# Kernel optimization log

Hardware: AMD Instinct MI355X
Metric: run time of the kernel (lower is better)

Reference implementation:

```python
import jax, jax.numpy as jnp
import numpy as np

PAST = 16
FUTURE = 4
DIM = 64
INPUT_SIZE = 256
NUM_LAYERS = 3
DILATION = [1, 2, 4, 8]
INPUT_LENGTH = 1024
BATCH = 16
NEG_INF = -1e9


def _dilated_masks(length, num_layers, dilation):
    # mask[i, t, s] == True means position t may NOT attend to position s in layer i.
    # Layer i attends to s = t - k*dilation[i] for k in [0, window) with
    # window = dilation[i+1] // dilation[i] (causal, dilated local window).
    idx = np.arange(length)
    diff = idx[:, None] - idx[None, :]  # t - s
    masks = []
    for i in range(num_layers):
        d = dilation[i]
        window = dilation[i + 1] // d
        allowed = (diff >= 0) & (diff % d == 0) & (diff < window * d)
        masks.append(~allowed)
    return jnp.asarray(np.stack(masks, 0))


def setup_inputs() -> dict:
    key = jax.random.key(0)
    k_inp, k_w, k_b = jax.random.split(key, 3)
    inp = jax.random.normal(k_inp, (BATCH, INPUT_LENGTH, INPUT_SIZE), dtype=jnp.float32)
    # BottleLinear(input_size, output_size): plain Linear over last dim
    out_size = FUTURE * DIM
    bound = 1.0 / np.sqrt(INPUT_SIZE)
    W_out = jax.random.uniform(k_w, (out_size, INPUT_SIZE), minval=-bound, maxval=bound, dtype=jnp.float32)
    b_out = jax.random.uniform(k_b, (out_size,), minval=-bound, maxval=bound, dtype=jnp.float32)
    masks = _dilated_masks(INPUT_LENGTH, NUM_LAYERS, DILATION)
    return {"inp": inp, "W_out": W_out, "b_out": b_out, "masks": masks}


def reference(inp, W_out, b_out, masks):
    # inp: [B, L, D]; masks: [num_layers, L, L] bool (True = masked)
    B, L, D = inp.shape
    scale = 1.0 / jnp.sqrt(jnp.asarray(D, inp.dtype))
    residual = inp[:, PAST:, :DIM][:, :, None, :]  # [B, L-past, 1, dim]
    out = inp
    attns = []
    for i in range(NUM_LAYERS):
        mask = masks[i, :L, :L]
        scores = jnp.einsum('bld,bmd->blm', out, out) * scale
        scores = jnp.where(mask[None], NEG_INF, scores)
        attn = jax.nn.softmax(scores, axis=-1)  # [B, L, L]
        # dropout=0.0 (eval); residual self-attention layer
        out = jnp.einsum('blm,bmd->bld', attn, out) + out
        attns.append(attn)
    o = out[:, PAST:]  # [B, L-past, D]
    o = jnp.einsum('bld,od->blo', o, W_out) + b_out
    o = o.reshape(B, L - PAST, FUTURE, DIM) + residual
    attn_stack = jnp.stack(attns, 1)  # [B, num_layers, L, L]
    return o, attn_stack
```

## Files before the change

### kernel.cpp

```cpp
#include <hip/hip_runtime.h>

#define BATCH 16
#define LEN 1024
#define DIN 256
#define PAST 16
#define OUTROWS (LEN - PAST)
#define NL 3
#define TROWS 32
#define HALO 8
#define NR (TROWS + HALO)
#define O_ELEMS ((size_t)BATCH * OUTROWS * 256)

typedef float f4_t __attribute__((ext_vector_type(4)));

__device__ __forceinline__ void layer_step(const float (*S)[DIN], float (*D)[DIN],
                                           const int DD, const int layer,
                                           const int b, const int l0,
                                           const int wave, const int lane,
                                           float* __restrict__ attn)
{
    #pragma unroll
    for (int it = 0; it < NR / 8; ++it) {
        const int row = it * 8 + wave;
        const int l   = l0 - HALO + row;
        const int ry  = (row >= DD) ? (row - DD) : 0;

        const float4 x = ((const float4*)(S[row]))[lane];
        const float4 y = ((const float4*)(S[ry]))[lane];

        float d0 = x.x * x.x + x.y * x.y + x.z * x.z + x.w * x.w;
        float d1 = x.x * y.x + x.y * y.y + x.z * y.z + x.w * y.w;
        #pragma unroll
        for (int off = 32; off; off >>= 1) {
            d0 += __shfl_xor(d0, off, 64);
            d1 += __shfl_xor(d1, off, 64);
        }

        float p0 = 1.f, p1 = 0.f;
        if (l >= DD) {
            const float s0 = d0 * 0.0625f, s1 = d1 * 0.0625f;
            const float m  = fmaxf(s0, s1);
            const float e0 = expf(s0 - m), e1 = expf(s1 - m);
            const float inv = 1.f / (e0 + e1);
            p0 = e0 * inv;
            p1 = e1 * inv;
        }

        const float a0 = 1.f + p0;
        float4 nv;
        nv.x = fmaf(y.x, p1, x.x * a0);
        nv.y = fmaf(y.y, p1, x.y * a0);
        nv.z = fmaf(y.z, p1, x.z * a0);
        nv.w = fmaf(y.w, p1, x.w * a0);
        ((float4*)(D[row]))[lane] = nv;

        if (row >= HALO) {
            float* arow = attn + (((size_t)(b * NL + layer)) * LEN + l) * (size_t)LEN;
            #pragma unroll
            for (int j = 0; j < 4; ++j) {
                const int col = j * 256 + lane * 4;
                float4 v = make_float4(0.f, 0.f, 0.f, 0.f);
                const int dd = l - col;
                if (dd >= 0 && dd < 4) ((float*)&v)[dd] = p0;
                if (l >= DD) {
                    const int dp = (l - DD) - col;
                    if (dp >= 0 && dp < 4) ((float*)&v)[dp] = p1;
                }
                __builtin_nontemporal_store(*(const f4_t*)&v,
                                            (f4_t*)arow + j * 64 + lane);
            }
        }
    }
}

__global__ __launch_bounds__(512, 4) void fused_kernel(const float* __restrict__ inp,
                                                       const float* __restrict__ W,
                                                       const float* __restrict__ bias,
                                                       float* __restrict__ o,
                                                       float* __restrict__ attn)
{
    __shared__ float A[NR][DIN];
    __shared__ float Bb[NR][DIN];

    const int blk  = blockIdx.x;
    const int b    = blk >> 5;
    const int l0   = (blk & 31) * TROWS;
    const int t    = threadIdx.x;
    const int wave = t >> 6;
    const int lane = t & 63;

    {
        float4* dst = (float4*)A;
        const size_t base = (size_t)b * LEN;
        #pragma unroll
        for (int i = 0; i < 5; ++i) {
            const int idx = i * 512 + t;
            const int row = idx >> 6;
            int g = l0 - HALO + row; if (g < 0) g = 0;
            dst[idx] = ((const float4*)(inp + (base + g) * DIN))[idx & 63];
        }
    }
    __syncthreads();

    layer_step(A,  Bb, 1, 0, b, l0, wave, lane, attn);
    __syncthreads();
    layer_step(Bb, A,  2, 1, b, l0, wave, lane, attn);
    __syncthreads();
    layer_step(A,  Bb, 4, 2, b, l0, wave, lane, attn);
    __syncthreads();

    const int half = t >> 8;
    const int c    = t & 255;
    float acc[16];
    #pragma unroll
    for (int r = 0; r < 16; ++r) acc[r] = 0.f;

    const float4* W4 = (const float4*)(W + (size_t)c * DIN);
    const float4* R4 = (const float4*)(Bb[HALO + half * 16]);
    for (int kq = 0; kq < 64; ++kq) {
        const float4 wv = W4[kq];
        #pragma unroll
        for (int r = 0; r < 16; ++r) {
            const float4 xr = R4[r * 64 + kq];
            acc[r] = fmaf(wv.x, xr.x, acc[r]);
            acc[r] = fmaf(wv.y, xr.y, acc[r]);
            acc[r] = fmaf(wv.z, xr.z, acc[r]);
            acc[r] = fmaf(wv.w, xr.w, acc[r]);
        }
    }

    const float bv   = bias[c];
    const int   dcol = c & 63;
    #pragma unroll
    for (int r = 0; r < 16; ++r) {
        const int l = l0 + half * 16 + r;
        if (l >= PAST) {
            const float res = inp[((size_t)b * LEN + l) * DIN + dcol];
            o[((size_t)b * OUTROWS + (l - PAST)) * 256 + c] = acc[r] + bv + res;
        }
    }
}

extern "C" void kernel_launch(void* const* d_in, const int* in_sizes, int n_in,
                              void* d_out, int out_size, void* d_ws, size_t ws_size,
                              hipStream_t stream) {
    const float* inp   = (const float*)d_in[0];
    const float* W_out = (const float*)d_in[1];
    const float* b_out = (const float*)d_in[2];

    float* o_out    = (float*)d_out;
    float* attn_out = o_out + O_ELEMS;

    fused_kernel<<<BATCH * (LEN / TROWS), 512, 0, stream>>>(inp, W_out, b_out,
                                                            o_out, attn_out);
}
```

Before: 303.6 us.

## Drop final barrier and retile output projection so each wave owns its rows

Turns layer_step into a template with compile-time dilation, layer and row range, and skips the first row group of the last layer because those halo rows feed no output. The output linear is retiled so each wave computes a 4-row by 4-column block only from rows it wrote itself. That lets the final __syncthreads be removed, and the output is written with vectorized non-temporal float4 stores. The cost is strided W loads across lanes (each lane reads four separate W rows), which may hurt coalescing compared with the old contiguous per-thread row reads.

After: 403.2 us. 32.8% more time.

```diff
diff --git a/kernel.cpp b/kernel.cpp
--- a/kernel.cpp
+++ b/kernel.cpp
@@ -13,14 +13,14 @@
 
 typedef float f4_t __attribute__((ext_vector_type(4)));
 
+template<int DD, int LAYER, int ITBEG, int ITEND>
 __device__ __forceinline__ void layer_step(const float (*S)[DIN], float (*D)[DIN],
-                                           const int DD, const int layer,
                                            const int b, const int l0,
                                            const int wave, const int lane,
                                            float* __restrict__ attn)
 {
     #pragma unroll
-    for (int it = 0; it < NR / 8; ++it) {
+    for (int it = ITBEG; it < ITEND; ++it) {
         const int row = it * 8 + wave;
         const int l   = l0 - HALO + row;
         const int ry  = (row >= DD) ? (row - DD) : 0;
@@ -55,7 +55,7 @@
         ((float4*)(D[row]))[lane] = nv;
 
         if (row >= HALO) {
-            float* arow = attn + (((size_t)(b * NL + layer)) * LEN + l) * (size_t)LEN;
+            float* arow = attn + (((size_t)(b * NL + LAYER)) * LEN + l) * (size_t)LEN;
             #pragma unroll
             for (int j = 0; j < 4; ++j) {
                 const int col = j * 256 + lane * 4;
@@ -102,41 +102,53 @@
     }
     __syncthreads();
 
-    layer_step(A,  Bb, 1, 0, b, l0, wave, lane, attn);
+    layer_step<1, 0, 0, 5>(A,  Bb, b, l0, wave, lane, attn);
     __syncthreads();
-    layer_step(Bb, A,  2, 1, b, l0, wave, lane, attn);
+    layer_step<2, 1, 0, 5>(Bb, A,  b, l0, wave, lane, attn);
     __syncthreads();
-    layer_step(A,  Bb, 4, 2, b, l0, wave, lane, attn);
-    __syncthreads();
+    layer_step<4, 2, 1, 5>(A,  Bb, b, l0, wave, lane, attn);
 
-    const int half = t >> 8;
-    const int c    = t & 255;
-    float acc[16];
+    float acc[4][4];
     #pragma unroll
-    for (int r = 0; r < 16; ++r) acc[r] = 0.f;
+    for (int q = 0; q < 4; ++q)
+        #pragma unroll
+        for (int j = 0; j < 4; ++j) acc[q][j] = 0.f;
 
-    const float4* W4 = (const float4*)(W + (size_t)c * DIN);
-    const float4* R4 = (const float4*)(Bb[HALO + half * 16]);
+    const float4* W4 = (const float4*)W;
+    const int c0 = 4 * lane;
     for (int kq = 0; kq < 64; ++kq) {
-        const float4 wv = W4[kq];
+        float4 x[4];
         #pragma unroll
-        for (int r = 0; r < 16; ++r) {
-            const float4 xr = R4[r * 64 + kq];
-            acc[r] = fmaf(wv.x, xr.x, acc[r]);
-            acc[r] = fmaf(wv.y, xr.y, acc[r]);
-            acc[r] = fmaf(wv.z, xr.z, acc[r]);
-            acc[r] = fmaf(wv.w, xr.w, acc[r]);
+        for (int q = 0; q < 4; ++q)
+            x[q] = ((const float4*)(Bb[HALO + wave + 8 * q]))[kq];
+        float4 wr[4];
+        #pragma unroll
+        for (int j = 0; j < 4; ++j)
+            wr[j] = W4[(size_t)(c0 + j) * 64 + kq];
+        #pragma unroll
+        for (int q = 0; q < 4; ++q) {
+            #pragma unroll
+            for (int j = 0; j < 4; ++j) {
+                acc[q][j] += x[q].x * wr[j].x + x[q].y * wr[j].y
+                           + x[q].z * wr[j].z + x[q].w * wr[j].w;
+            }
         }
     }
 
-    const float bv   = bias[c];
-    const int   dcol = c & 63;
+    const float4 bv = ((const float4*)bias)[lane];
     #pragma unroll
-    for (int r = 0; r < 16; ++r) {
-        const int l = l0 + half * 16 + r;
+    for (int q = 0; q < 4; ++q) {
+        const int l = l0 + wave + 8 * q;
         if (l >= PAST) {
-            const float res = inp[((size_t)b * LEN + l) * DIN + dcol];
-            o[((size_t)b * OUTROWS + (l - PAST)) * 256 + c] = acc[r] + bv + res;
+            const float* irow = inp + ((size_t)b * LEN + l) * DIN;
+            const float4 rv = *(const float4*)(irow + (c0 & 63));
+            f4_t ov;
+            ov.x = acc[q][0] + bv.x + rv.x;
+            ov.y = acc[q][1] + bv.y + rv.y;
+            ov.z = acc[q][2] + bv.z + rv.z;
+            ov.w = acc[q][3] + bv.w + rv.w;
+            __builtin_nontemporal_store(ov,
+                (f4_t*)(o + ((size_t)b * OUTROWS + (l - PAST)) * 256) + lane);
         }
     }
 }
```
